# Kernel tuning notes

Measured on AMD Instinct MI355X. Metric: run time of the kernel, lower is better.

Reference implementation:

```python
import jax, jax.numpy as jnp
import numpy as np

V, E = 50000, 300          # vocab, embedding dim (Word2Vec)
U1, U2, DNS = 256, 256, 128  # lstm1 units, lstm2 units, dense units
B, S = 64, 512             # batch, seq_len


def _glorot(key, shape):
    fan_in, fan_out = shape
    lim = jnp.sqrt(6.0 / (fan_in + fan_out))
    return jax.random.uniform(key, shape, jnp.float32, -lim, lim)


def setup_inputs() -> dict:
    key = jax.random.key(0)
    ks = jax.random.split(key, 12)
    d = {
        'tokens': jax.random.randint(ks[0], (B, S), 0, V),
        'emb': jax.random.normal(ks[1], (V, E), jnp.float32) * 0.05,
        # layer 1 gates: combined dim = E + U1
        'W1f': _glorot(ks[2], (E + U1, U1)), 'b1f': jnp.zeros((U1,), jnp.float32),
        'W1i': _glorot(ks[3], (E + U1, U1)), 'b1i': jnp.zeros((U1,), jnp.float32),
        'W1c': _glorot(ks[4], (E + U1, U1)), 'b1c': jnp.zeros((U1,), jnp.float32),
        'W1o': _glorot(ks[5], (E + U1, U1)), 'b1o': jnp.zeros((U1,), jnp.float32),
        # layer 2 gates: combined dim = U1 + U2
        'W2f': _glorot(ks[6], (U1 + U2, U2)), 'b2f': jnp.zeros((U2,), jnp.float32),
        'W2i': _glorot(ks[7], (U1 + U2, U2)), 'b2i': jnp.zeros((U2,), jnp.float32),
        'W2c': _glorot(ks[8], (U1 + U2, U2)), 'b2c': jnp.zeros((U2,), jnp.float32),
        'W2o': _glorot(ks[9], (U1 + U2, U2)), 'b2o': jnp.zeros((U2,), jnp.float32),
        'Wd': _glorot(ks[10], (U2, DNS)), 'bd': jnp.zeros((DNS,), jnp.float32),
        'Wout': _glorot(ks[11], (DNS, 1)), 'bout': jnp.zeros((1,), jnp.float32),
    }
    return d


def _lstm(x_seq, Wf, bf, Wi, bi, Wc, bc, Wo, bo, units):
    # x_seq: [B, S, D]; scan over time, returns all hidden states [B, S, units]
    b = x_seq.shape[0]
    h0 = jnp.zeros((b, units), x_seq.dtype)
    c0 = jnp.zeros((b, units), x_seq.dtype)

    def step(carry, x_t):
        h, c = carry
        z = jnp.concatenate([x_t, h], axis=-1)           # [B, D+units]
        f = jax.nn.sigmoid(z @ Wf + bf)
        i = jax.nn.sigmoid(z @ Wi + bi)
        g = jnp.tanh(z @ Wc + bc)
        c_new = f * c + i * g
        o = jax.nn.sigmoid(z @ Wo + bo)
        h_new = o * jnp.tanh(c_new)
        return (h_new, c_new), h_new

    (_, _), hs = jax.lax.scan(step, (h0, c0), jnp.swapaxes(x_seq, 0, 1))
    return jnp.swapaxes(hs, 0, 1)  # [B, S, units]


def reference(tokens, emb, W1f, b1f, W1i, b1i, W1c, b1c, W1o, b1o,
              W2f, b2f, W2i, b2i, W2c, b2c, W2o, b2o, Wd, bd, Wout, bout):
    x = emb[tokens]                                       # [B, S, E]
    h1 = _lstm(x, W1f, b1f, W1i, b1i, W1c, b1c, W1o, b1o, U1)   # [B, S, U1]
    h2 = _lstm(h1, W2f, b2f, W2i, b2i, W2c, b2c, W2o, b2o, U2)  # [B, S, U2]
    last = h2[:, -1, :]                                   # return_sequences=False -> final h
    d = jax.nn.relu(last @ Wd + bd)
    return jax.nn.sigmoid(d @ Wout + bout)                # [B, 1]
```

## Files before the change

### kernel.cpp

```cpp
#include <hip/hip_runtime.h>
#include <stdint.h>

typedef __bf16 bf16_t;
typedef __bf16 bf16x8 __attribute__((ext_vector_type(8)));
typedef float floatx16 __attribute__((ext_vector_type(16)));
typedef unsigned int u32;
typedef unsigned long long u64;

#define NPROD 64
#define H1R   8
#define SST   592
#define ZST   1104
#define FP    32

struct KParams {
  const int* tok;
  const float* emb;
  const float* W1[4]; const float* b1[4];
  const float* W2[4]; const float* b2[4];
  const float* Wd; const float* bd; const float* Wout; const float* bout;
  float* out;
  uint16_t* h1;
  uint16_t* h2;
  u32* fl0;
  u32* fl1;
  u32* fl0g;
  u32* pflags;
  float* dstage;
  bf16_t* w1bf;
  float* gx;
  int R;
};

__device__ __forceinline__ float sigf(float x) { return 1.f / (1.f + __expf(-x)); }
__device__ __forceinline__ float tanhf_fast(float x) { return 1.f - 2.f / (__expf(2.f * x) + 1.f); }

__device__ __forceinline__ u32 pack2(float a, float b) {
  uint16_t x = __builtin_bit_cast(uint16_t, (bf16_t)a);
  uint16_t y = __builtin_bit_cast(uint16_t, (bf16_t)b);
  return ((u32)y << 16) | (u32)x;
}
__device__ __forceinline__ float2 u2f2(u64 v) { union { u64 u; float2 f; } x; x.u = v; return x.f; }

__device__ __forceinline__ u32  ald32(const u32* p) { return __hip_atomic_load(p, __ATOMIC_RELAXED, __HIP_MEMORY_SCOPE_AGENT); }
__device__ __forceinline__ void ast32(u32* p, u32 v) { __hip_atomic_store(p, v, __ATOMIC_RELAXED, __HIP_MEMORY_SCOPE_AGENT); }
__device__ __forceinline__ u64  ald64(const u64* p) { return __hip_atomic_load(p, __ATOMIC_RELAXED, __HIP_MEMORY_SCOPE_AGENT); }

template<int NA, int NB>
__device__ __forceinline__ void waitcond(const u32* fa, u32 na, const u32* fb, u32 nb,
                                         const u32* pc, u32 nc) {
  const int lane = threadIdx.x & 63;
  const u32* ap; u32 need;
  if (lane < NA)           { ap = fa + lane * FP;        need = na; }
  else if (lane < NA + NB) { ap = fb + (lane - NA) * FP; need = nb; }
  else                     { ap = pc;                    need = nc; }
  while (!__all(ald32(ap) >= need)) {}
  __atomic_signal_fence(__ATOMIC_ACQUIRE);
}

__device__ __forceinline__ void waitg16(const u32* fa, u32 na) {
  const int lane = threadIdx.x & 63;
  const u32* ap = fa + (lane & 15) * FP;
  while (!__all(ald32(ap) >= na)) {}
  __atomic_signal_fence(__ATOMIC_ACQUIRE);
}

__device__ __forceinline__ void stage_h64(const u64* hp, char* smem) {
  const int tid = threadIdx.x;
  u64 tmp[16];
#pragma unroll
  for (int t = 0; t < 16; ++t) tmp[t] = ald64(hp + tid + 256 * t);
#pragma unroll
  for (int t = 0; t < 16; ++t) {
    int i = tid + 256 * t, b = i >> 6, cc = i & 63;
    *(u64*)(smem + b * SST + cc * 8) = tmp[t];
  }
}

__device__ void run_l0(const KParams& p, int sub, char* abuf, float* cst, float* biasl)
{
  const int tid = threadIdx.x;
  const int w = tid >> 6, l = tid & 63, q = l >> 5, lr = l & 31;
  const int mh = w & 1, nh = w >> 1;

  if (tid < 64) biasl[tid] = p.b1[tid >> 4][sub * 16 + (tid & 15)];

  const int c = nh * 32 + lr;
  const float* Wg = p.W1[c >> 4];
  const int un = sub * 16 + (c & 15);
  bf16x8 wf[16];
#pragma unroll
  for (int s = 0; s < 16; ++s)
#pragma unroll
    for (int j = 0; j < 8; ++j) {
      int k = 16 * s + 8 * q + j;
      wf[s][j] = (bf16_t)Wg[(300 + k) * 256 + un];
    }
  __syncthreads();

  float cs[2][2] = {{0.f, 0.f}, {0.f, 0.f}};

  for (int s = 0; s < 512; ++s) {
    u32 n1 = (s >= 8) ? (u32)(s - 7) : 0u;
    if (w == 0) waitcond<16, 32>(p.fl0, (u32)s, p.fl1, n1, &p.pflags[s * FP], 1u);
    __syncthreads();

    const float* slab = p.gx + (size_t)(s % p.R) * 65536u;
    u64 g[2][4];
#pragma unroll
    for (int kk = 0; kk < 2; ++kk) {
      int pp = tid + 256 * kk, b = pp >> 3, u2 = (pp & 7) * 2;
      const float* gb = slab + b * 1024 + sub * 64 + u2;
      g[kk][0] = ald64((const u64*)gb);
      g[kk][1] = ald64((const u64*)(gb + 16));
      g[kk][2] = ald64((const u64*)(gb + 32));
      g[kk][3] = ald64((const u64*)(gb + 48));
    }
    stage_h64((const u64*)(p.h1 + ((s + H1R - 1) & (H1R - 1)) * 16384), abuf);
    __syncthreads();

    floatx16 acc;
#pragma unroll
    for (int e = 0; e < 16; ++e) acc[e] = 0.f;
    const char* arow = abuf + (mh * 32 + lr) * SST + q * 16;
#pragma unroll
    for (int s2 = 0; s2 < 16; ++s2) {
      bf16x8 af = *(const bf16x8*)(arow + 32 * s2);
      acc = __builtin_amdgcn_mfma_f32_32x32x16_bf16(af, wf[s2], acc, 0, 0, 0);
    }
#pragma unroll
    for (int e = 0; e < 16; ++e) {
      int ri = (e & 3) + 8 * (e >> 2) + 4 * q;
      cst[(mh * 32 + ri) * 68 + nh * 32 + lr] = acc[e];
    }
    __syncthreads();

    uint16_t* hout = p.h1 + (s & (H1R - 1)) * 16384;
#pragma unroll
    for (int kk = 0; kk < 2; ++kk) {
      int pp = tid + 256 * kk, b = pp >> 3, u2 = (pp & 7) * 2;
      float2 pf = *(float2*)&cst[b * 68 +      u2];
      float2 pi = *(float2*)&cst[b * 68 + 16 + u2];
      float2 pg = *(float2*)&cst[b * 68 + 32 + u2];
      float2 po = *(float2*)&cst[b * 68 + 48 + u2];
      float2 gf = u2f2(g[kk][0]), gi = u2f2(g[kk][1]);
      float2 gg = u2f2(g[kk][2]), go = u2f2(g[kk][3]);
      float hv[2];
#pragma unroll
      for (int j = 0; j < 2; ++j) {
        float fj = sigf((j ? pf.y : pf.x) + (j ? gf.y : gf.x) + biasl[u2 + j]);
        float ij = sigf((j ? pi.y : pi.x) + (j ? gi.y : gi.x) + biasl[16 + u2 + j]);
        float gj = tanhf_fast((j ? pg.y : pg.x) + (j ? gg.y : gg.x) + biasl[32 + u2 + j]);
        float oj = sigf((j ? po.y : po.x) + (j ? go.y : go.x) + biasl[48 + u2 + j]);
        float cn = fj * cs[kk][j] + ij * gj;
        cs[kk][j] = cn;
        hv[j] = oj * tanhf_fast(cn);
      }
      ast32((u32*)(hout + b * 256 + sub * 16 + u2), pack2(hv[0], hv[1]));
    }
    __syncthreads();
    if (tid == 0) {
      ast32(&p.fl0[sub * FP], (u32)(s + 1));
      ast32(&p.fl0g[sub * FP], (u32)(s + 1));
    }
  }
}

__device__ void run_l1(const KParams& p, int w2, char* zbuf, float* cst, float* biasl)
{
  const int tid = threadIdx.x;
  const int wv = tid >> 6, l = tid & 63, q = l >> 5, lr = l & 31;
  const int nh = wv & 1, kh = wv >> 1;
  const int bh = w2 & 1, sub1 = w2 >> 1;

  if (tid < 64) biasl[tid] = p.b2[tid >> 4][sub1 * 16 + (tid & 15)];

  const int c = nh * 32 + lr;
  const float* Wg = p.W2[c >> 4];
  const int un = sub1 * 16 + (c & 15);
  bf16x8 wf[16];
#pragma unroll
  for (int s = 0; s < 16; ++s)
#pragma unroll
    for (int j = 0; j < 8; ++j) {
      int k = kh * 256 + s * 16 + q * 8 + j;
      wf[s][j] = (bf16_t)Wg[k * 256 + un];
    }
  __syncthreads();

  float cs2[2] = {0.f, 0.f};
  const int cb = tid >> 3, cu = (tid & 7) * 2;

  for (int s = 0; s < 512; ++s) {
    if (wv == 0) waitcond<32, 16>(p.fl1, (u32)s, p.fl0, (u32)(s + 1), p.fl0, 0u);
    __syncthreads();

    const u64* hp1 = (const u64*)(p.h1 + (s & (H1R - 1)) * 16384) + bh * 2048;
    const u64* hp2 = (const u64*)(p.h2 + ((s + 1) & 1) * 16384) + bh * 2048;
    u64 t1[8], t2[8];
#pragma unroll
    for (int t = 0; t < 8; ++t) t1[t] = ald64(hp1 + tid + 256 * t);
#pragma unroll
    for (int t = 0; t < 8; ++t) t2[t] = ald64(hp2 + tid + 256 * t);
#pragma unroll
    for (int t = 0; t < 8; ++t) {
      int i = tid + 256 * t, r = i >> 6, cc = i & 63;
      *(u64*)(zbuf + r * ZST + cc * 8) = t1[t];
    }
#pragma unroll
    for (int t = 0; t < 8; ++t) {
      int i = tid + 256 * t, r = i >> 6, cc = i & 63;
      *(u64*)(zbuf + r * ZST + 512 + cc * 8) = t2[t];
    }
    __syncthreads();

    floatx16 acc;
#pragma unroll
    for (int e = 0; e < 16; ++e) acc[e] = 0.f;
    const char* arow = zbuf + lr * ZST + kh * 512 + q * 16;
#pragma unroll
    for (int s2 = 0; s2 < 16; ++s2) {
      bf16x8 af = *(const bf16x8*)(arow + 32 * s2);
      acc = __builtin_amdgcn_mfma_f32_32x32x16_bf16(af, wf[s2], acc, 0, 0, 0);
    }
#pragma unroll
    for (int e = 0; e < 16; ++e) {
      int ri = (e & 3) + 8 * (e >> 2) + 4 * q;
      cst[kh * 2176 + ri * 68 + nh * 32 + lr] = acc[e];
    }
    __syncthreads();

    uint16_t* hout = p.h2 + (s & 1) * 16384;
    {
      float2 pf = *(float2*)&cst[cb * 68 +      cu];
      float2 pi = *(float2*)&cst[cb * 68 + 16 + cu];
      float2 pg = *(float2*)&cst[cb * 68 + 32 + cu];
      float2 po = *(float2*)&cst[cb * 68 + 48 + cu];
      float2 qf = *(float2*)&cst[2176 + cb * 68 +      cu];
      float2 qi = *(float2*)&cst[2176 + cb * 68 + 16 + cu];
      float2 qg = *(float2*)&cst[2176 + cb * 68 + 32 + cu];
      float2 qo = *(float2*)&cst[2176 + cb * 68 + 48 + cu];
      float hv[2];
#pragma unroll
      for (int j = 0; j < 2; ++j) {
        float fj = sigf((j ? pf.y + qf.y : pf.x + qf.x) + biasl[cu + j]);
        float ij = sigf((j ? pi.y + qi.y : pi.x + qi.x) + biasl[16 + cu + j]);
        float gj = tanhf_fast((j ? pg.y + qg.y : pg.x + qg.x) + biasl[32 + cu + j]);
        float oj = sigf((j ? po.y + qo.y : po.x + qo.x) + biasl[48 + cu + j]);
        float cn = fj * cs2[j] + ij * gj;
        cs2[j] = cn;
        hv[j] = oj * tanhf_fast(cn);
      }
      ast32((u32*)(hout + (bh * 32 + cb) * 256 + sub1 * 16 + cu), pack2(hv[0], hv[1]));
    }
    __syncthreads();
    if (tid == 0) ast32(&p.fl1[w2 * FP], (u32)(s + 1));
  }

  if (wv == 0) waitcond<32, 0>(p.fl1, 512u, p.fl1, 0u, p.fl1, 0u);
  __syncthreads();
  {
    const u64* hp = (const u64*)(p.h2 + 16384);
    u64 tmp[16];
#pragma unroll
    for (int t = 0; t < 16; ++t) tmp[t] = ald64(hp + tid + 256 * t);
#pragma unroll
    for (int t = 0; t < 16; ++t) {
      int i = tid + 256 * t, b = i >> 6, cc = i & 63;
      *(u64*)(zbuf + b * 520 + cc * 8) = tmp[t];
    }
  }
  __syncthreads();
  {
    int b = tid >> 2, cc = w2 * 4 + (tid & 3);
    const bf16_t* hrow = (const bf16_t*)(zbuf + b * 520);
    float a = p.bd[cc];
#pragma unroll 8
    for (int k = 0; k < 256; ++k) a += (float)hrow[k] * p.Wd[k * 128 + cc];
    ast32((u32*)&p.dstage[b * 128 + cc], __builtin_bit_cast(u32, fmaxf(a, 0.f)));
  }
  __syncthreads();
  if (tid == 0) ast32(&p.fl1[w2 * FP], 513u);

  if (w2 == 0) {
    if (wv == 0) waitcond<32, 0>(p.fl1, 513u, p.fl1, 0u, p.fl1, 0u);
    __syncthreads();
    if (tid < 64) {
      float a = p.bout[0];
#pragma unroll 8
      for (int cc = 0; cc < 128; ++cc) {
        u32 dv = ald32((u32*)&p.dstage[tid * 128 + cc]);
        a += __builtin_bit_cast(float, dv) * p.Wout[cc];
      }
      p.out[tid] = sigf(a);
    }
  }
}

__device__ void run_prod(const KParams& p, int pw, char* smem)
{
  const int tid = threadIdx.x;
  const int w = tid >> 6, l = tid & 63, q = l >> 5, lr = l & 31;
  const int mh = w & 1, chalf = w >> 1;
  const int R = p.R;

  for (int jj = 0; jj < 512 / NPROD; ++jj) {
    const int s = pw + NPROD * jj;
    if (s >= R) {
      if (w == 0) waitg16(p.fl0g, (u32)(s - R + 1));
    }
    __syncthreads();
    {
      int b = tid >> 2, qq = tid & 3;
      int tokv = p.tok[b * 512 + s];
      const float4* src = (const float4*)(p.emb + (size_t)tokv * 300);
      char* dst = smem + b * 656;
      for (int j2 = qq; j2 < 75; j2 += 4) {
        float4 v = src[j2];
        *(u32*)(dst + 8 * j2)     = pack2(v.x, v.y);
        *(u32*)(dst + 8 * j2 + 4) = pack2(v.z, v.w);
      }
      for (int i = tid; i < 640; i += 256) {
        int bb = i / 10, cc2 = i % 10;
        *(u32*)(smem + bb * 656 + 600 + cc2 * 4) = 0u;
      }
    }
    __syncthreads();

    bf16x8 afr[20];
    const char* arow = smem + (mh * 32 + lr) * 656 + q * 16;
#pragma unroll
    for (int kt = 0; kt < 20; ++kt) afr[kt] = *(const bf16x8*)(arow + 32 * kt);

    float* slab = p.gx + (size_t)(s % R) * 65536u;
    for (int c2 = 0; c2 < 16; ++c2) {
      int n = (chalf * 16 + c2) * 32 + lr;
      floatx16 acc;
#pragma unroll
      for (int e = 0; e < 16; ++e) acc[e] = 0.f;
#pragma unroll
      for (int kt = 0; kt < 20; ++kt) {
        bf16x8 bf = ((const bf16x8*)p.w1bf)[(kt * 1024 + n) * 2 + q];
        acc = __builtin_amdgcn_mfma_f32_32x32x16_bf16(afr[kt], bf, acc, 0, 0, 0);
      }
#pragma unroll
      for (int e = 0; e < 16; ++e) {
        int ri = (e & 3) + 8 * (e >> 2) + 4 * q;
        ast32((u32*)(slab + (mh * 32 + ri) * 1024 + n), __builtin_bit_cast(u32, acc[e]));
      }
    }
    __syncthreads();
    if (tid == 0) ast32(&p.pflags[s * FP], 1u);
  }
}

__global__ __launch_bounds__(256, 1) void lstm_main(KParams p)
{
  __shared__ __align__(16) char smem[64 * 656];
  __shared__ float cst[4352];
  __shared__ float biasl[64];
  const int wg = blockIdx.x;
  if (wg < 16)       run_l0(p, wg, smem, cst, biasl);
  else if (wg < 48)  run_l1(p, wg - 16, smem, cst, biasl);
  else               run_prod(p, wg - 48, smem);
}

__global__ void prep_w(KParams p) {
  int idx = blockIdx.x * 256 + threadIdx.x;
  if (idx >= 20 * 1024 * 16) return;
  int kk = idx & 15, n = (idx >> 4) & 1023, kt = idx >> 14;
  int k = kt * 16 + kk;
  int g = (n >> 4) & 3, su = n >> 6, u = n & 15;
  float v = (k < 300) ? p.W1[g][k * 256 + su * 16 + u] : 0.f;
  p.w1bf[idx] = (bf16_t)v;
}

__global__ void init_ws(u32* ws32) {
  int i = blockIdx.x * 256 + threadIdx.x;
  if (i < 100352) ws32[i] = 0u;
}

extern "C" void kernel_launch(void* const* d_in, const int* in_sizes, int n_in,
                              void* d_out, int out_size, void* d_ws, size_t ws_size,
                              hipStream_t stream)
{
  KParams p;
  p.tok = (const int*)d_in[0];
  p.emb = (const float*)d_in[1];
  for (int g = 0; g < 4; ++g) {
    p.W1[g] = (const float*)d_in[2 + 2 * g];
    p.b1[g] = (const float*)d_in[3 + 2 * g];
    p.W2[g] = (const float*)d_in[10 + 2 * g];
    p.b2[g] = (const float*)d_in[11 + 2 * g];
  }
  p.Wd   = (const float*)d_in[18];
  p.bd   = (const float*)d_in[19];
  p.Wout = (const float*)d_in[20];
  p.bout = (const float*)d_in[21];
  p.out  = (float*)d_out;

  char* ws = (char*)d_ws;
  p.h1     = (uint16_t*)ws;
  p.h2     = (uint16_t*)(ws + 262144);
  p.fl0    = (u32*)(ws + 327680);
  p.fl1    = (u32*)(ws + 329728);
  p.fl0g   = (u32*)(ws + 333824);
  p.pflags = (u32*)(ws + 335872);
  p.dstage = (float*)(ws + 401408);
  p.w1bf   = (bf16_t*)(ws + 434176);
  p.gx     = (float*)(ws + 1089536);

  long avail = (long)ws_size - 1089536L;
  int R = (int)(avail / 262144L);
  if (R > 64) R = 64;
  if (R < 1)  R = 1;
  p.R = R;

  hipLaunchKernelGGL(init_ws, dim3(392), dim3(256), 0, stream, (u32*)d_ws);
  hipLaunchKernelGGL(prep_w, dim3(1280), dim3(256), 0, stream, p);
  hipLaunchKernelGGL(lstm_main, dim3(16 + 32 + NPROD), dim3(256), 0, stream, p);
}
```

Before: 1.860 ms.

## Use per-wave progress flags and prefetch h1 to overlap LSTM layer steps

Each wavefront now publishes its own progress flag after draining its stores with s_waitcnt. This replaces the block-wide __syncthreads plus single-thread flag store. Consumers poll all the relevant flags with wave-level min reductions or __all loops, and gx readiness is tracked incrementally with a ballot scan. Layer 2 splits its K loop so the h1 half of the MFMA runs before waiting on the h2 flags, and it prefetches the next step's h1 into registers, shortening the critical path of the serial recurrence. The cost is four times as many flag slots, more polling traffic, and subtler memory-ordering assumptions.

```diff
diff --git a/kernel.cpp b/kernel.cpp
--- a/kernel.cpp
+++ b/kernel.cpp
@@ -20,8 +20,8 @@
   const float* W2[4]; const float* b2[4];
   const float* Wd; const float* bd; const float* Wout; const float* bout;
   float* out;
-  uint16_t* h1;
-  uint16_t* h2;
+  u64* h1;
+  u64* h2;
   u32* fl0;
   u32* fl1;
   u32* fl0g;
@@ -46,35 +46,24 @@
 __device__ __forceinline__ void ast32(u32* p, u32 v) { __hip_atomic_store(p, v, __ATOMIC_RELAXED, __HIP_MEMORY_SCOPE_AGENT); }
 __device__ __forceinline__ u64  ald64(const u64* p) { return __hip_atomic_load(p, __ATOMIC_RELAXED, __HIP_MEMORY_SCOPE_AGENT); }
 
-template<int NA, int NB>
-__device__ __forceinline__ void waitcond(const u32* fa, u32 na, const u32* fb, u32 nb,
-                                         const u32* pc, u32 nc) {
-  const int lane = threadIdx.x & 63;
-  const u32* ap; u32 need;
-  if (lane < NA)           { ap = fa + lane * FP;        need = na; }
-  else if (lane < NA + NB) { ap = fb + (lane - NA) * FP; need = nb; }
-  else                     { ap = pc;                    need = nc; }
-  while (!__all(ald32(ap) >= need)) {}
-  __atomic_signal_fence(__ATOMIC_ACQUIRE);
-}
-
-__device__ __forceinline__ void waitg16(const u32* fa, u32 na) {
-  const int lane = threadIdx.x & 63;
-  const u32* ap = fa + (lane & 15) * FP;
-  while (!__all(ald32(ap) >= na)) {}
-  __atomic_signal_fence(__ATOMIC_ACQUIRE);
-}
-
-__device__ __forceinline__ void stage_h64(const u64* hp, char* smem) {
-  const int tid = threadIdx.x;
-  u64 tmp[16];
-#pragma unroll
-  for (int t = 0; t < 16; ++t) tmp[t] = ald64(hp + tid + 256 * t);
-#pragma unroll
-  for (int t = 0; t < 16; ++t) {
-    int i = tid + 256 * t, b = i >> 6, cc = i & 63;
-    *(u64*)(smem + b * SST + cc * 8) = tmp[t];
-  }
+__device__ __forceinline__ void vdrain() {
+  asm volatile("s_waitcnt vmcnt(0)" ::: "memory");
+  __builtin_amdgcn_sched_barrier(0);
+}
+
+__device__ __forceinline__ u32 wmin(u32 f) {
+#pragma unroll
+  for (int d = 1; d < 64; d <<= 1) { u32 o = (u32)__shfl_xor((int)f, d); f = o < f ? o : f; }
+  return f;
+}
+
+__device__ __forceinline__ void gx_scan(const KParams& p, int l, int& gxok) {
+  int base = gxok + 1;
+  u32 ok = 0u;
+  if (l < 16) { int idx = base + l; ok = (idx >= 512) ? 1u : (ald32(p.pflags + (size_t)idx * FP) ? 1u : 0u); }
+  u64 m = __ballot(ok != 0u);
+  int t = (int)__builtin_ctzll(~m);
+  gxok = base + t - 1;
 }
 
 __device__ void run_l0(const KParams& p, int sub, char* abuf, float* cst, float* biasl)
@@ -90,20 +79,24 @@
   const int un = sub * 16 + (c & 15);
   bf16x8 wf[16];
 #pragma unroll
-  for (int s = 0; s < 16; ++s)
-#pragma unroll
-    for (int j = 0; j < 8; ++j) {
-      int k = 16 * s + 8 * q + j;
-      wf[s][j] = (bf16_t)Wg[(300 + k) * 256 + un];
-    }
+  for (int s2 = 0; s2 < 16; ++s2)
+#pragma unroll
+    for (int j = 0; j < 8; ++j)
+      wf[s2][j] = (bf16_t)Wg[(300 + 16 * s2 + 8 * q + j) * 256 + un];
   __syncthreads();
 
   float cs[2][2] = {{0.f, 0.f}, {0.f, 0.f}};
+  int gxok = -1, ringok = 0;
 
   for (int s = 0; s < 512; ++s) {
-    u32 n1 = (s >= 8) ? (u32)(s - 7) : 0u;
-    if (w == 0) waitcond<16, 32>(p.fl0, (u32)s, p.fl1, n1, &p.pflags[s * FP], 1u);
-    __syncthreads();
+    while (ringok < s - 7) {
+      u32 a = ald32(p.fl1 + l * FP), b = ald32(p.fl1 + (l + 64) * FP);
+      ringok = (int)wmin(a < b ? a : b);
+    }
+    while (gxok < s) gx_scan(p, l, gxok);
+
+    for (;;) { u32 f = ald32(p.fl0 + l * FP); if (__all(f >= (u32)s)) break; }
+    __atomic_signal_fence(__ATOMIC_ACQUIRE);
 
     const float* slab = p.gx + (size_t)(s % p.R) * 65536u;
     u64 g[2][4];
@@ -116,7 +109,17 @@
       g[kk][2] = ald64((const u64*)(gb + 32));
       g[kk][3] = ald64((const u64*)(gb + 48));
     }
-    stage_h64((const u64*)(p.h1 + ((s + H1R - 1) & (H1R - 1)) * 16384), abuf);
+    {
+      const u64* hp = p.h1 + (size_t)((s + H1R - 1) & (H1R - 1)) * 4096;
+      u64 tmp[16];
+#pragma unroll
+      for (int t = 0; t < 16; ++t) tmp[t] = ald64(hp + tid + 256 * t);
+#pragma unroll
+      for (int t = 0; t < 16; ++t) {
+        int i = tid + 256 * t, b = i >> 6, cc = i & 63;
+        *(u64*)(abuf + b * SST + cc * 8) = tmp[t];
+      }
+    }
     __syncthreads();
 
     floatx16 acc;
@@ -135,7 +138,7 @@
     }
     __syncthreads();
 
-    uint16_t* hout = p.h1 + (s & (H1R - 1)) * 16384;
+    uint16_t* hout = (uint16_t*)(p.h1 + (size_t)(s & (H1R - 1)) * 4096);
 #pragma unroll
     for (int kk = 0; kk < 2; ++kk) {
       int pp = tid + 256 * kk, b = pp >> 3, u2 = (pp & 7) * 2;
@@ -158,10 +161,10 @@
       }
       ast32((u32*)(hout + b * 256 + sub * 16 + u2), pack2(hv[0], hv[1]));
     }
-    __syncthreads();
-    if (tid == 0) {
-      ast32(&p.fl0[sub * FP], (u32)(s + 1));
-      ast32(&p.fl0g[sub * FP], (u32)(s + 1));
+    vdrain();
+    if (l == 0) {
+      ast32(p.fl0  + (sub * 4 + w) * FP, (u32)(s + 1));
+      ast32(p.fl0g + (sub * 4 + w) * FP, (u32)(s + 1));
     }
   }
 }
@@ -170,7 +173,7 @@
 {
   const int tid = threadIdx.x;
   const int wv = tid >> 6, l = tid & 63, q = l >> 5, lr = l & 31;
-  const int nh = wv & 1, kh = wv >> 1;
+  const int nh = wv & 1, q4 = wv >> 1;
   const int bh = w2 & 1, sub1 = w2 >> 1;
 
   if (tid < 64) biasl[tid] = p.b2[tid >> 4][sub1 * 16 + (tid & 15)];
@@ -180,57 +183,74 @@
   const int un = sub1 * 16 + (c & 15);
   bf16x8 wf[16];
 #pragma unroll
-  for (int s = 0; s < 16; ++s)
+  for (int s2 = 0; s2 < 8; ++s2)
 #pragma unroll
     for (int j = 0; j < 8; ++j) {
-      int k = kh * 256 + s * 16 + q * 8 + j;
-      wf[s][j] = (bf16_t)Wg[k * 256 + un];
+      wf[s2][j]     = (bf16_t)Wg[(      q4 * 128 + s2 * 16 + q * 8 + j) * 256 + un];
+      wf[8 + s2][j] = (bf16_t)Wg[(256 + q4 * 128 + s2 * 16 + q * 8 + j) * 256 + un];
     }
   __syncthreads();
 
   float cs2[2] = {0.f, 0.f};
   const int cb = tid >> 3, cu = (tid & 7) * 2;
+  const int gidx = (2 * (l >> 2) + bh) * 4 + (l & 3);
+
+  int h1ok = -1;
+  while (h1ok < 0) { u32 f = ald32(p.fl0 + l * FP); h1ok = (int)wmin(f) - 1; }
+  __atomic_signal_fence(__ATOMIC_ACQUIRE);
+  u64 t1[8];
+  {
+    const u64* hp1 = p.h1 + bh * 2048;
+#pragma unroll
+    for (int t = 0; t < 8; ++t) t1[t] = ald64(hp1 + tid + 256 * t);
+  }
 
   for (int s = 0; s < 512; ++s) {
-    if (wv == 0) waitcond<32, 16>(p.fl1, (u32)s, p.fl0, (u32)(s + 1), p.fl0, 0u);
-    __syncthreads();
-
-    const u64* hp1 = (const u64*)(p.h1 + (s & (H1R - 1)) * 16384) + bh * 2048;
-    const u64* hp2 = (const u64*)(p.h2 + ((s + 1) & 1) * 16384) + bh * 2048;
-    u64 t1[8], t2[8];
-#pragma unroll
-    for (int t = 0; t < 8; ++t) t1[t] = ald64(hp1 + tid + 256 * t);
-#pragma unroll
-    for (int t = 0; t < 8; ++t) t2[t] = ald64(hp2 + tid + 256 * t);
 #pragma unroll
     for (int t = 0; t < 8; ++t) {
       int i = tid + 256 * t, r = i >> 6, cc = i & 63;
       *(u64*)(zbuf + r * ZST + cc * 8) = t1[t];
     }
-#pragma unroll
-    for (int t = 0; t < 8; ++t) {
-      int i = tid + 256 * t, r = i >> 6, cc = i & 63;
-      *(u64*)(zbuf + r * ZST + 512 + cc * 8) = t2[t];
-    }
     __syncthreads();
 
     floatx16 acc;
 #pragma unroll
     for (int e = 0; e < 16; ++e) acc[e] = 0.f;
-    const char* arow = zbuf + lr * ZST + kh * 512 + q * 16;
-#pragma unroll
-    for (int s2 = 0; s2 < 16; ++s2) {
-      bf16x8 af = *(const bf16x8*)(arow + 32 * s2);
+    const char* arow1 = zbuf + lr * ZST + q4 * 256 + q * 16;
+#pragma unroll
+    for (int s2 = 0; s2 < 8; ++s2) {
+      bf16x8 af = *(const bf16x8*)(arow1 + 32 * s2);
       acc = __builtin_amdgcn_mfma_f32_32x32x16_bf16(af, wf[s2], acc, 0, 0, 0);
+    }
+
+    for (;;) { u32 f = ald32(p.fl1 + gidx * FP); if (__all(f >= (u32)s)) break; }
+    __atomic_signal_fence(__ATOMIC_ACQUIRE);
+    {
+      const u64* hp2 = p.h2 + (size_t)((s + 1) & 1) * 4096 + bh * 2048;
+      u64 t2[8];
+#pragma unroll
+      for (int t = 0; t < 8; ++t) t2[t] = ald64(hp2 + tid + 256 * t);
+#pragma unroll
+      for (int t = 0; t < 8; ++t) {
+        int i = tid + 256 * t, r = i >> 6, cc = i & 63;
+        *(u64*)(zbuf + r * ZST + 512 + cc * 8) = t2[t];
+      }
+    }
+    __syncthreads();
+
+    const char* arow2 = zbuf + lr * ZST + 512 + q4 * 256 + q * 16;
+#pragma unroll
+    for (int s2 = 0; s2 < 8; ++s2) {
+      bf16x8 af = *(const bf16x8*)(arow2 + 32 * s2);
+      acc = __builtin_amdgcn_mfma_f32_32x32x16_bf16(af, wf[8 + s2], acc, 0, 0, 0);
     }
 #pragma unroll
     for (int e = 0; e < 16; ++e) {
       int ri = (e & 3) + 8 * (e >> 2) + 4 * q;
-      cst[kh * 2176 + ri * 68 + nh * 32 + lr] = acc[e];
-    }
-    __syncthreads();
-
-    uint16_t* hout = p.h2 + (s & 1) * 16384;
+      cst[q4 * 2176 + ri * 68 + nh * 32 + lr] = acc[e];
+    }
+    __syncthreads();
+
     {
       float2 pf = *(float2*)&cst[cb * 68 +      cu];
       float2 pi = *(float2*)&cst[cb * 68 + 16 + cu];
@@ -251,16 +271,27 @@
         cs2[j] = cn;
         hv[j] = oj * tanhf_fast(cn);
       }
+      uint16_t* hout = (uint16_t*)(p.h2 + (size_t)(s & 1) * 4096);
       ast32((u32*)(hout + (bh * 32 + cb) * 256 + sub1 * 16 + cu), pack2(hv[0], hv[1]));
     }
-    __syncthreads();
-    if (tid == 0) ast32(&p.fl1[w2 * FP], (u32)(s + 1));
-  }
-
-  if (wv == 0) waitcond<32, 0>(p.fl1, 512u, p.fl1, 0u, p.fl1, 0u);
-  __syncthreads();
+    vdrain();
+    if (l == 0) ast32(p.fl1 + (w2 * 4 + wv) * FP, (u32)(s + 1));
+
+    if (s < 511) {
+      while (h1ok < s + 1) { u32 f = ald32(p.fl0 + l * FP); h1ok = (int)wmin(f) - 1; }
+      const u64* hpn = p.h1 + (size_t)((s + 1) & (H1R - 1)) * 4096 + bh * 2048;
+#pragma unroll
+      for (int t = 0; t < 8; ++t) t1[t] = ald64(hpn + tid + 256 * t);
+    }
+  }
+
+  for (;;) {
+    u32 a = ald32(p.fl1 + l * FP), b = ald32(p.fl1 + (l + 64) * FP);
+    if (__all((a >= 512u) && (b >= 512u))) break;
+  }
+  __atomic_signal_fence(__ATOMIC_ACQUIRE);
   {
-    const u64* hp = (const u64*)(p.h2 + 16384);
+    const u64* hp = p.h2 + 4096;
     u64 tmp[16];
 #pragma unroll
     for (int t = 0; t < 16; ++t) tmp[t] = ald64(hp + tid + 256 * t);
@@ -279,12 +310,15 @@
     for (int k = 0; k < 256; ++k) a += (float)hrow[k] * p.Wd[k * 128 + cc];
     ast32((u32*)&p.dstage[b * 128 + cc], __builtin_bit_cast(u32, fmaxf(a, 0.f)));
   }
-  __syncthreads();
-  if (tid == 0) ast32(&p.fl1[w2 * FP], 513u);
+  vdrain();
+  if (l == 0) ast32(p.fl1 + (w2 * 4 + wv) * FP, 600u);
 
   if (w2 == 0) {
-    if (wv == 0) waitcond<32, 0>(p.fl1, 513u, p.fl1, 0u, p.fl1, 0u);
-    __syncthreads();
+    for (;;) {
+      u32 a = ald32(p.fl1 + l * FP), b = ald32(p.fl1 + (l + 64) * FP);
+      if (__all((a >= 600u) && (b >= 600u))) break;
+    }
+    __atomic_signal_fence(__ATOMIC_ACQUIRE);
     if (tid < 64) {
       float a = p.bout[0];
 #pragma unroll 8
@@ -307,7 +341,11 @@
   for (int jj = 0; jj < 512 / NPROD; ++jj) {
     const int s = pw + NPROD * jj;
     if (s >= R) {
-      if (w == 0) waitg16(p.fl0g, (u32)(s - R + 1));
+      if (w == 0) {
+        u32 need = (u32)(s - R + 1);
+        for (;;) { u32 f = ald32(p.fl0g + l * FP); if (__all(f >= need)) break; }
+        __atomic_signal_fence(__ATOMIC_ACQUIRE);
+      }
     }
     __syncthreads();
     {
@@ -350,7 +388,7 @@
       }
     }
     __syncthreads();
-    if (tid == 0) ast32(&p.pflags[s * FP], 1u);
+    if (tid == 0) ast32(&p.pflags[(size_t)s * FP], 1u);
   }
 }
 
@@ -377,7 +415,7 @@
 
 __global__ void init_ws(u32* ws32) {
   int i = blockIdx.x * 256 + threadIdx.x;
-  if (i < 100352) ws32[i] = 0u;
+  if (i < 106496) ws32[i] = 0u;
 }
 
 extern "C" void kernel_launch(void* const* d_in, const int* in_sizes, int n_in,
@@ -400,23 +438,23 @@
   p.out  = (float*)d_out;
 
   char* ws = (char*)d_ws;
-  p.h1     = (uint16_t*)ws;
-  p.h2     = (uint16_t*)(ws + 262144);
+  p.h1     = (u64*)ws;
+  p.h2     = (u64*)(ws + 262144);
   p.fl0    = (u32*)(ws + 327680);
-  p.fl1    = (u32*)(ws + 329728);
-  p.fl0g   = (u32*)(ws + 333824);
-  p.pflags = (u32*)(ws + 335872);
-  p.dstage = (float*)(ws + 401408);
-  p.w1bf   = (bf16_t*)(ws + 434176);
-  p.gx     = (float*)(ws + 1089536);
-
-  long avail = (long)ws_size - 1089536L;
+  p.fl1    = (u32*)(ws + 335872);
+  p.fl0g   = (u32*)(ws + 352256);
+  p.pflags = (u32*)(ws + 360448);
+  p.dstage = (float*)(ws + 425984);
+  p.w1bf   = (bf16_t*)(ws + 458752);
+  p.gx     = (float*)(ws + 1114112);
+
+  long avail = (long)ws_size - 1114112L;
   int R = (int)(avail / 262144L);
   if (R > 64) R = 64;
   if (R < 1)  R = 1;
   p.R = R;
 
-  hipLaunchKernelGGL(init_ws, dim3(392), dim3(256), 0, stream, (u32*)d_ws);
+  hipLaunchKernelGGL(init_ws, dim3(416), dim3(256), 0, stream, (u32*)d_ws);
   hipLaunchKernelGGL(prep_w, dim3(1280), dim3(256), 0, stream, p);
   hipLaunchKernelGGL(lstm_main, dim3(16 + 32 + NPROD), dim3(256), 0, stream, p);
 }
```

Measured after the change: 2.340 ms. 1.26x slower.

## Halve persistent workgroup counts with 512-thread blocks per LSTM stage

Applied to the files above, without the earlier changes.

Block size doubles from 256 to 512 threads, and the recurrence workgroups are halved: layer-1 goes from 16 to 8 and layer-2 from 32 to 16. Each workgroup now owns 32 hidden units, and producers drop from 64 to 32. Fewer workgroups means fewer cross-workgroup flag waits per timestep, so the inter-block synchronisation on the serial recurrence gets cheaper. In exchange each block does twice the MFMA and staging work per step. The partial-sum buffer now aliases the shared staging buffer, which needs an extra barrier.

```diff
diff --git a/kernel.cpp b/kernel.cpp
--- a/kernel.cpp
+++ b/kernel.cpp
@@ -7,7 +7,7 @@
 typedef unsigned int u32;
 typedef unsigned long long u64;
 
-#define NPROD 64
+#define NPROD 32
 #define H1R   8
 #define SST   592
 #define ZST   1104
@@ -20,8 +20,8 @@
   const float* W2[4]; const float* b2[4];
   const float* Wd; const float* bd; const float* Wout; const float* bout;
   float* out;
-  uint16_t* h1;
-  uint16_t* h2;
+  u64* h1;
+  u64* h2;
   u32* fl0;
   u32* fl1;
   u32* fl0g;
@@ -58,105 +58,98 @@
   __atomic_signal_fence(__ATOMIC_ACQUIRE);
 }
 
-__device__ __forceinline__ void waitg16(const u32* fa, u32 na) {
-  const int lane = threadIdx.x & 63;
-  const u32* ap = fa + (lane & 15) * FP;
-  while (!__all(ald32(ap) >= na)) {}
-  __atomic_signal_fence(__ATOMIC_ACQUIRE);
-}
-
-__device__ __forceinline__ void stage_h64(const u64* hp, char* smem) {
-  const int tid = threadIdx.x;
-  u64 tmp[16];
-#pragma unroll
-  for (int t = 0; t < 16; ++t) tmp[t] = ald64(hp + tid + 256 * t);
-#pragma unroll
-  for (int t = 0; t < 16; ++t) {
-    int i = tid + 256 * t, b = i >> 6, cc = i & 63;
-    *(u64*)(smem + b * SST + cc * 8) = tmp[t];
-  }
-}
-
-__device__ void run_l0(const KParams& p, int sub, char* abuf, float* cst, float* biasl)
+__device__ void run_l0(const KParams& p, int sub, char* smem, float* biasl)
 {
   const int tid = threadIdx.x;
   const int w = tid >> 6, l = tid & 63, q = l >> 5, lr = l & 31;
-  const int mh = w & 1, nh = w >> 1;
-
-  if (tid < 64) biasl[tid] = p.b1[tid >> 4][sub * 16 + (tid & 15)];
-
-  const int c = nh * 32 + lr;
-  const float* Wg = p.W1[c >> 4];
-  const int un = sub * 16 + (c & 15);
+  const int mh = w & 1, nq = w >> 1;
+  float* cst = (float*)smem;
+
+  if (tid < 128) biasl[tid] = p.b1[tid >> 5][sub * 32 + (tid & 31)];
+
+  const int cc = nq * 32 + lr;
+  const int su = 2 * sub + (cc >> 6);
+  const float* Wg = p.W1[(cc >> 4) & 3];
+  const int un = su * 16 + (cc & 15);
   bf16x8 wf[16];
 #pragma unroll
-  for (int s = 0; s < 16; ++s)
-#pragma unroll
-    for (int j = 0; j < 8; ++j) {
-      int k = 16 * s + 8 * q + j;
-      wf[s][j] = (bf16_t)Wg[(300 + k) * 256 + un];
-    }
+  for (int s2 = 0; s2 < 16; ++s2)
+#pragma unroll
+    for (int j = 0; j < 8; ++j)
+      wf[s2][j] = (bf16_t)Wg[(300 + 16 * s2 + 8 * q + j) * 256 + un];
   __syncthreads();
 
   float cs[2][2] = {{0.f, 0.f}, {0.f, 0.f}};
 
   for (int s = 0; s < 512; ++s) {
     u32 n1 = (s >= 8) ? (u32)(s - 7) : 0u;
-    if (w == 0) waitcond<16, 32>(p.fl0, (u32)s, p.fl1, n1, &p.pflags[s * FP], 1u);
+    if (w == 0) waitcond<8, 16>(p.fl0, (u32)s, p.fl1, n1, &p.pflags[(size_t)s * FP], 1u);
     __syncthreads();
 
     const float* slab = p.gx + (size_t)(s % p.R) * 65536u;
     u64 g[2][4];
 #pragma unroll
     for (int kk = 0; kk < 2; ++kk) {
-      int pp = tid + 256 * kk, b = pp >> 3, u2 = (pp & 7) * 2;
-      const float* gb = slab + b * 1024 + sub * 64 + u2;
+      int pp = tid + 512 * kk, b = pp >> 4, u2 = (pp & 15) * 2;
+      const float* gb = slab + b * 1024 + (2 * sub + (u2 >> 4)) * 64 + (u2 & 15);
       g[kk][0] = ald64((const u64*)gb);
       g[kk][1] = ald64((const u64*)(gb + 16));
       g[kk][2] = ald64((const u64*)(gb + 32));
       g[kk][3] = ald64((const u64*)(gb + 48));
     }
-    stage_h64((const u64*)(p.h1 + ((s + H1R - 1) & (H1R - 1)) * 16384), abuf);
+    {
+      const u64* hp = p.h1 + (size_t)((s + H1R - 1) & (H1R - 1)) * 4096;
+      u64 tmp[8];
+#pragma unroll
+      for (int t = 0; t < 8; ++t) tmp[t] = ald64(hp + tid + 512 * t);
+#pragma unroll
+      for (int t = 0; t < 8; ++t) {
+        int i = tid + 512 * t, b = i >> 6, c2 = i & 63;
+        *(u64*)(smem + b * SST + c2 * 8) = tmp[t];
+      }
+    }
     __syncthreads();
 
     floatx16 acc;
 #pragma unroll
     for (int e = 0; e < 16; ++e) acc[e] = 0.f;
-    const char* arow = abuf + (mh * 32 + lr) * SST + q * 16;
+    const char* arow = smem + (mh * 32 + lr) * SST + q * 16;
 #pragma unroll
     for (int s2 = 0; s2 < 16; ++s2) {
       bf16x8 af = *(const bf16x8*)(arow + 32 * s2);
       acc = __builtin_amdgcn_mfma_f32_32x32x16_bf16(af, wf[s2], acc, 0, 0, 0);
     }
+    __syncthreads();
 #pragma unroll
     for (int e = 0; e < 16; ++e) {
       int ri = (e & 3) + 8 * (e >> 2) + 4 * q;
-      cst[(mh * 32 + ri) * 68 + nh * 32 + lr] = acc[e];
-    }
-    __syncthreads();
-
-    uint16_t* hout = p.h1 + (s & (H1R - 1)) * 16384;
+      cst[(mh * 32 + ri) * 132 + nq * 32 + lr] = acc[e];
+    }
+    __syncthreads();
+
+    uint16_t* hout = (uint16_t*)(p.h1 + (size_t)(s & (H1R - 1)) * 4096);
 #pragma unroll
     for (int kk = 0; kk < 2; ++kk) {
-      int pp = tid + 256 * kk, b = pp >> 3, u2 = (pp & 7) * 2;
-      float2 pf = *(float2*)&cst[b * 68 +      u2];
-      float2 pi = *(float2*)&cst[b * 68 + 16 + u2];
-      float2 pg = *(float2*)&cst[b * 68 + 32 + u2];
-      float2 po = *(float2*)&cst[b * 68 + 48 + u2];
+      int pp = tid + 512 * kk, b = pp >> 4, u2 = (pp & 15) * 2;
+      int base = b * 132 + (u2 >> 4) * 64 + (u2 & 15);
+      float2 pf = *(float2*)&cst[base];
+      float2 pi = *(float2*)&cst[base + 16];
+      float2 pg = *(float2*)&cst[base + 32];
+      float2 po = *(float2*)&cst[base + 48];
       float2 gf = u2f2(g[kk][0]), gi = u2f2(g[kk][1]);
       float2 gg = u2f2(g[kk][2]), go = u2f2(g[kk][3]);
       float hv[2];
 #pragma unroll
       for (int j = 0; j < 2; ++j) {
         float fj = sigf((j ? pf.y : pf.x) + (j ? gf.y : gf.x) + biasl[u2 + j]);
-        float ij = sigf((j ? pi.y : pi.x) + (j ? gi.y : gi.x) + biasl[16 + u2 + j]);
-        float gj = tanhf_fast((j ? pg.y : pg.x) + (j ? gg.y : gg.x) + biasl[32 + u2 + j]);
-        float oj = sigf((j ? po.y : po.x) + (j ? go.y : go.x) + biasl[48 + u2 + j]);
+        float ij = sigf((j ? pi.y : pi.x) + (j ? gi.y : gi.x) + biasl[32 + u2 + j]);
+        float gj = tanhf_fast((j ? pg.y : pg.x) + (j ? gg.y : gg.x) + biasl[64 + u2 + j]);
+        float oj = sigf((j ? po.y : po.x) + (j ? go.y : go.x) + biasl[96 + u2 + j]);
         float cn = fj * cs[kk][j] + ij * gj;
         cs[kk][j] = cn;
         hv[j] = oj * tanhf_fast(cn);
       }
-      ast32((u32*)(hout + b * 256 + sub * 16 + u2), pack2(hv[0], hv[1]));
+      ast32((u32*)(hout + b * 256 + sub * 32 + u2), pack2(hv[0], hv[1]));
     }
     __syncthreads();
     if (tid == 0) {
@@ -166,51 +159,51 @@
   }
 }
 
-__device__ void run_l1(const KParams& p, int w2, char* zbuf, float* cst, float* biasl)
+__device__ void run_l1(const KParams& p, int w2, char* zbuf, float* biasl)
 {
   const int tid = threadIdx.x;
   const int wv = tid >> 6, l = tid & 63, q = l >> 5, lr = l & 31;
-  const int nh = wv & 1, kh = wv >> 1;
-  const int bh = w2 & 1, sub1 = w2 >> 1;
-
-  if (tid < 64) biasl[tid] = p.b2[tid >> 4][sub1 * 16 + (tid & 15)];
-
-  const int c = nh * 32 + lr;
-  const float* Wg = p.W2[c >> 4];
-  const int un = sub1 * 16 + (c & 15);
+  const int nq = wv & 3, kh = wv >> 2;
+  const int bh = w2 & 1, subq = w2 >> 1;
+  float* cst = (float*)zbuf;
+
+  if (tid < 128) biasl[tid] = p.b2[tid >> 5][subq * 32 + (tid & 31)];
+
+  const int cc = nq * 32 + lr;
+  const int su = 2 * subq + (cc >> 6);
+  const float* Wg = p.W2[(cc >> 4) & 3];
+  const int un = su * 16 + (cc & 15);
   bf16x8 wf[16];
 #pragma unroll
-  for (int s = 0; s < 16; ++s)
-#pragma unroll
-    for (int j = 0; j < 8; ++j) {
-      int k = kh * 256 + s * 16 + q * 8 + j;
-      wf[s][j] = (bf16_t)Wg[k * 256 + un];
-    }
+  for (int s2 = 0; s2 < 16; ++s2)
+#pragma unroll
+    for (int j = 0; j < 8; ++j)
+      wf[s2][j] = (bf16_t)Wg[(kh * 256 + 16 * s2 + 8 * q + j) * 256 + un];
   __syncthreads();
 
   float cs2[2] = {0.f, 0.f};
-  const int cb = tid >> 3, cu = (tid & 7) * 2;
+  const int cb = tid >> 4, cu = (tid & 15) * 2;
 
   for (int s = 0; s < 512; ++s) {
-    if (wv == 0) waitcond<32, 16>(p.fl1, (u32)s, p.fl0, (u32)(s + 1), p.fl0, 0u);
-    __syncthreads();
-
-    const u64* hp1 = (const u64*)(p.h1 + (s & (H1R - 1)) * 16384) + bh * 2048;
-    const u64* hp2 = (const u64*)(p.h2 + ((s + 1) & 1) * 16384) + bh * 2048;
-    u64 t1[8], t2[8];
-#pragma unroll
-    for (int t = 0; t < 8; ++t) t1[t] = ald64(hp1 + tid + 256 * t);
-#pragma unroll
-    for (int t = 0; t < 8; ++t) t2[t] = ald64(hp2 + tid + 256 * t);
-#pragma unroll
-    for (int t = 0; t < 8; ++t) {
-      int i = tid + 256 * t, r = i >> 6, cc = i & 63;
-      *(u64*)(zbuf + r * ZST + cc * 8) = t1[t];
-    }
-#pragma unroll
-    for (int t = 0; t < 8; ++t) {
-      int i = tid + 256 * t, r = i >> 6, cc = i & 63;
-      *(u64*)(zbuf + r * ZST + 512 + cc * 8) = t2[t];
+    if (wv == 0) waitcond<16, 8>(p.fl1, (u32)s, p.fl0, (u32)(s + 1), p.fl1, 0u);
+    __syncthreads();
+
+    const u64* hp1 = p.h1 + (size_t)(s & (H1R - 1)) * 4096 + bh * 2048;
+    const u64* hp2 = p.h2 + (size_t)((s + 1) & 1) * 4096 + bh * 2048;
+    u64 t1[4], t2[4];
+#pragma unroll
+    for (int t = 0; t < 4; ++t) t1[t] = ald64(hp1 + tid + 512 * t);
+#pragma unroll
+    for (int t = 0; t < 4; ++t) t2[t] = ald64(hp2 + tid + 512 * t);
+#pragma unroll
+    for (int t = 0; t < 4; ++t) {
+      int i = tid + 512 * t, r = i >> 6, c2 = i & 63;
+      *(u64*)(zbuf + r * ZST + c2 * 8) = t1[t];
+    }
+#pragma unroll
+    for (int t = 0; t < 4; ++t) {
+      int i = tid + 512 * t, r = i >> 6, c2 = i & 63;
+      *(u64*)(zbuf + r * ZST + 512 + c2 * 8) = t2[t];
     }
     __syncthreads();
 
@@ -223,74 +216,76 @@
       bf16x8 af = *(const bf16x8*)(arow + 32 * s2);
       acc = __builtin_amdgcn_mfma_f32_32x32x16_bf16(af, wf[s2], acc, 0, 0, 0);
     }
+    __syncthreads();
 #pragma unroll
     for (int e = 0; e < 16; ++e) {
       int ri = (e & 3) + 8 * (e >> 2) + 4 * q;
-      cst[kh * 2176 + ri * 68 + nh * 32 + lr] = acc[e];
-    }
-    __syncthreads();
-
-    uint16_t* hout = p.h2 + (s & 1) * 16384;
+      cst[kh * 4224 + ri * 132 + nq * 32 + lr] = acc[e];
+    }
+    __syncthreads();
+
     {
-      float2 pf = *(float2*)&cst[cb * 68 +      cu];
-      float2 pi = *(float2*)&cst[cb * 68 + 16 + cu];
-      float2 pg = *(float2*)&cst[cb * 68 + 32 + cu];
-      float2 po = *(float2*)&cst[cb * 68 + 48 + cu];
-      float2 qf = *(float2*)&cst[2176 + cb * 68 +      cu];
-      float2 qi = *(float2*)&cst[2176 + cb * 68 + 16 + cu];
-      float2 qg = *(float2*)&cst[2176 + cb * 68 + 32 + cu];
-      float2 qo = *(float2*)&cst[2176 + cb * 68 + 48 + cu];
+      int base = cb * 132 + (cu >> 4) * 64 + (cu & 15);
+      float2 pf = *(float2*)&cst[base];
+      float2 pi = *(float2*)&cst[base + 16];
+      float2 pg = *(float2*)&cst[base + 32];
+      float2 po = *(float2*)&cst[base + 48];
+      float2 qf = *(float2*)&cst[4224 + base];
+      float2 qi = *(float2*)&cst[4224 + base + 16];
+      float2 qg = *(float2*)&cst[4224 + base + 32];
+      float2 qo = *(float2*)&cst[4224 + base + 48];
       float hv[2];
 #pragma unroll
       for (int j = 0; j < 2; ++j) {
         float fj = sigf((j ? pf.y + qf.y : pf.x + qf.x) + biasl[cu + j]);
-        float ij = sigf((j ? pi.y + qi.y : pi.x + qi.x) + biasl[16 + cu + j]);
-        float gj = tanhf_fast((j ? pg.y + qg.y : pg.x + qg.x) + biasl[32 + cu + j]);
-        float oj = sigf((j ? po.y + qo.y : po.x + qo.x) + biasl[48 + cu + j]);
+        float ij = sigf((j ? pi.y + qi.y : pi.x + qi.x) + biasl[32 + cu + j]);
+        float gj = tanhf_fast((j ? pg.y + qg.y : pg.x + qg.x) + biasl[64 + cu + j]);
+        float oj = sigf((j ? po.y + qo.y : po.x + qo.x) + biasl[96 + cu + j]);
         float cn = fj * cs2[j] + ij * gj;
         cs2[j] = cn;
         hv[j] = oj * tanhf_fast(cn);
       }
-      ast32((u32*)(hout + (bh * 32 + cb) * 256 + sub1 * 16 + cu), pack2(hv[0], hv[1]));
+      uint16_t* hout = (uint16_t*)(p.h2 + (size_t)(s & 1) * 4096);
+      ast32((u32*)(hout + (bh * 32 + cb) * 256 + subq * 32 + cu), pack2(hv[0], hv[1]));
     }
     __syncthreads();
     if (tid == 0) ast32(&p.fl1[w2 * FP], (u32)(s + 1));
   }
 
-  if (wv == 0) waitcond<32, 0>(p.fl1, 512u, p.fl1, 0u, p.fl1, 0u);
+  if (wv == 0) waitcond<16, 0>(p.fl1, 512u, p.fl1, 0u, p.fl1, 0u);
   __syncthreads();
   {
-    const u64* hp = (const u64*)(p.h2 + 16384);
-    u64 tmp[16];
-#pragma unroll
-    for (int t = 0; t < 16; ++t) tmp[t] = ald64(hp + tid + 256 * t);
-#pragma unroll
-    for (int t = 0; t < 16; ++t) {
-      int i = tid + 256 * t, b = i >> 6, cc = i & 63;
-      *(u64*)(zbuf + b * 520 + cc * 8) = tmp[t];
+    const u64* hp = p.h2 + 4096;
+    u64 tmp[8];
+#pragma unroll
+    for (int t = 0; t < 8; ++t) tmp[t] = ald64(hp + tid + 512 * t);
+#pragma unroll
+    for (int t = 0; t < 8; ++t) {
+      int i = tid + 512 * t, b = i >> 6, c2 = i & 63;
+      *(u64*)(zbuf + b * 520 + c2 * 8) = tmp[t];
     }
   }
   __syncthreads();
   {
-    int b = tid >> 2, cc = w2 * 4 + (tid & 3);
+    int b = tid >> 3, cd = w2 * 8 + (tid & 7);
     const bf16_t* hrow = (const bf16_t*)(zbuf + b * 520);
-    float a = p.bd[cc];
+    float a = p.bd[cd];
 #pragma unroll 8
-    for (int k = 0; k < 256; ++k) a += (float)hrow[k] * p.Wd[k * 128 + cc];
-    ast32((u32*)&p.dstage[b * 128 + cc], __builtin_bit_cast(u32, fmaxf(a, 0.f)));
+    for (int k = 0; k < 256; ++k) a += (float)hrow[k] * p.Wd[k * 128 + cd];
+    ast32((u32*)&p.dstage[b * 128 + cd], __builtin_bit_cast(u32, fmaxf(a, 0.f)));
   }
   __syncthreads();
-  if (tid == 0) ast32(&p.fl1[w2 * FP], 513u);
+  if (tid == 0) ast32(&p.fl1[w2 * FP], 600u);
 
   if (w2 == 0) {
-    if (wv == 0) waitcond<32, 0>(p.fl1, 513u, p.fl1, 0u, p.fl1, 0u);
+    if (wv == 0) waitcond<16, 0>(p.fl1, 600u, p.fl1, 0u, p.fl1, 0u);
     __syncthreads();
     if (tid < 64) {
       float a = p.bout[0];
 #pragma unroll 8
-      for (int cc = 0; cc < 128; ++cc) {
-        u32 dv = ald32((u32*)&p.dstage[tid * 128 + cc]);
-        a += __builtin_bit_cast(float, dv) * p.Wout[cc];
+      for (int cd = 0; cd < 128; ++cd) {
+        u32 dv = ald32((u32*)&p.dstage[tid * 128 + cd]);
+        a += __builtin_bit_cast(float, dv) * p.Wout[cd];
       }
       p.out[tid] = sigf(a);
     }
@@ -301,28 +296,28 @@
 {
   const int tid = threadIdx.x;
   const int w = tid >> 6, l = tid & 63, q = l >> 5, lr = l & 31;
-  const int mh = w & 1, chalf = w >> 1;
+  const int mh = w & 1, nq = w >> 1;
   const int R = p.R;
 
   for (int jj = 0; jj < 512 / NPROD; ++jj) {
     const int s = pw + NPROD * jj;
     if (s >= R) {
-      if (w == 0) waitg16(p.fl0g, (u32)(s - R + 1));
+      if (w == 0) waitcond<8, 0>(p.fl0g, (u32)(s - R + 1), p.fl0g, 0u, p.fl0g, 0u);
     }
     __syncthreads();
     {
-      int b = tid >> 2, qq = tid & 3;
+      int b = tid >> 3, qq = tid & 7;
       int tokv = p.tok[b * 512 + s];
       const float4* src = (const float4*)(p.emb + (size_t)tokv * 300);
       char* dst = smem + b * 656;
-      for (int j2 = qq; j2 < 75; j2 += 4) {
+      for (int j2 = qq; j2 < 75; j2 += 8) {
         float4 v = src[j2];
         *(u32*)(dst + 8 * j2)     = pack2(v.x, v.y);
         *(u32*)(dst + 8 * j2 + 4) = pack2(v.z, v.w);
       }
-      for (int i = tid; i < 640; i += 256) {
-        int bb = i / 10, cc2 = i % 10;
-        *(u32*)(smem + bb * 656 + 600 + cc2 * 4) = 0u;
+      for (int i = tid; i < 640; i += 512) {
+        int bb = i / 10, c2 = i % 10;
+        *(u32*)(smem + bb * 656 + 600 + c2 * 4) = 0u;
       }
     }
     __syncthreads();
@@ -333,8 +328,8 @@
     for (int kt = 0; kt < 20; ++kt) afr[kt] = *(const bf16x8*)(arow + 32 * kt);
 
     float* slab = p.gx + (size_t)(s % R) * 65536u;
-    for (int c2 = 0; c2 < 16; ++c2) {
-      int n = (chalf * 16 + c2) * 32 + lr;
+    for (int c2 = 0; c2 < 8; ++c2) {
+      int n = (nq * 8 + c2) * 32 + lr;
       floatx16 acc;
 #pragma unroll
       for (int e = 0; e < 16; ++e) acc[e] = 0.f;
@@ -350,19 +345,18 @@
       }
     }
     __syncthreads();
-    if (tid == 0) ast32(&p.pflags[s * FP], 1u);
-  }
-}
-
-__global__ __launch_bounds__(256, 1) void lstm_main(KParams p)
+    if (tid == 0) ast32(&p.pflags[(size_t)s * FP], 1u);
+  }
+}
+
+__global__ __launch_bounds__(512, 1) void lstm_main(KParams p)
 {
   __shared__ __align__(16) char smem[64 * 656];
-  __shared__ float cst[4352];
-  __shared__ float biasl[64];
+  __shared__ float biasl[128];
   const int wg = blockIdx.x;
-  if (wg < 16)       run_l0(p, wg, smem, cst, biasl);
-  else if (wg < 48)  run_l1(p, wg - 16, smem, cst, biasl);
-  else               run_prod(p, wg - 48, smem);
+  if (wg < 8)        run_l0(p, wg, smem, biasl);
+  else if (wg < 24)  run_l1(p, wg - 8, smem, biasl);
+  else               run_prod(p, wg - 24, smem);
 }
 
 __global__ void prep_w(KParams p) {
@@ -377,7 +371,7 @@
 
 __global__ void init_ws(u32* ws32) {
   int i = blockIdx.x * 256 + threadIdx.x;
-  if (i < 100352) ws32[i] = 0u;
+  if (i < 99328) ws32[i] = 0u;
 }
 
 extern "C" void kernel_launch(void* const* d_in, const int* in_sizes, int n_in,
@@ -400,23 +394,23 @@
   p.out  = (float*)d_out;
 
   char* ws = (char*)d_ws;
-  p.h1     = (uint16_t*)ws;
-  p.h2     = (uint16_t*)(ws + 262144);
+  p.h1     = (u64*)ws;
+  p.h2     = (u64*)(ws + 262144);
   p.fl0    = (u32*)(ws + 327680);
-  p.fl1    = (u32*)(ws + 329728);
-  p.fl0g   = (u32*)(ws + 333824);
-  p.pflags = (u32*)(ws + 335872);
-  p.dstage = (float*)(ws + 401408);
-  p.w1bf   = (bf16_t*)(ws + 434176);
-  p.gx     = (float*)(ws + 1089536);
-
-  long avail = (long)ws_size - 1089536L;
+  p.fl1    = (u32*)(ws + 328704);
+  p.fl0g   = (u32*)(ws + 330752);
+  p.pflags = (u32*)(ws + 331776);
+  p.dstage = (float*)(ws + 397312);
+  p.w1bf   = (bf16_t*)(ws + 430080);
+  p.gx     = (float*)(ws + 1085440);
+
+  long avail = (long)ws_size - 1085440L;
   int R = (int)(avail / 262144L);
   if (R > 64) R = 64;
   if (R < 1)  R = 1;
   p.R = R;
 
-  hipLaunchKernelGGL(init_ws, dim3(392), dim3(256), 0, stream, (u32*)d_ws);
+  hipLaunchKernelGGL(init_ws, dim3(388), dim3(256), 0, stream, (u32*)d_ws);
   hipLaunchKernelGGL(prep_w, dim3(1280), dim3(256), 0, stream, p);
-  hipLaunchKernelGGL(lstm_main, dim3(16 + 32 + NPROD), dim3(256), 0, stream, p);
-}
+  hipLaunchKernelGGL(lstm_main, dim3(8 + 16 + NPROD), dim3(512), 0, stream, p);
+}
```

New measurement: 2.378 ms. +27.8%, slower.
